# Optimization experiments

Hardware: AMD Instinct MI355X
Metric: run time of the kernel (lower is better)

## Reference

```python
import jax, jax.numpy as jnp
import numpy as np

EPS = 1e-4  # performer softmax-kernel stabilizer
LN_EPS = 1e-5


def _layernorm(x, g, b):
    m = jnp.mean(x, axis=-1, keepdims=True)
    v = jnp.mean(jnp.square(x - m), axis=-1, keepdims=True)
    return (x - m) * jax.lax.rsqrt(v + LN_EPS) * g + b


def _softmax_features(x, proj, is_query):
    # FAVOR+ positive softmax-kernel features. x: [B,H,N,Dh], proj: [M,Dh]
    d = x.shape[-1]
    xn = x * (d ** -0.25)                      # data normalizer d^{-1/4}
    u = jnp.einsum('bhnd,md->bhnm', xn, proj)  # [B,H,N,M]
    diag = 0.5 * jnp.sum(jnp.square(xn), axis=-1, keepdims=True)
    if is_query:
        stab = jnp.max(u, axis=-1, keepdims=True)
    else:
        stab = jnp.max(u, axis=(-2, -1), keepdims=True)
    ratio = proj.shape[0] ** -0.5
    return ratio * (jnp.exp(u - diag - stab) + EPS)


def reference(x, proj, ln1_g, ln1_b, ln2_g, ln2_b, W1, b1, W2, b2):
    B, N, E = x.shape
    M, Dh = proj.shape
    H = E // Dh

    # --- multi-head fast attention sublayer (pre-LN, q=k=v, no dropout) ---
    h = _layernorm(x, ln1_g, ln1_b)
    qkv = h.reshape(B, N, H, Dh).transpose(0, 2, 1, 3)     # [B,H,N,Dh]
    q_p = _softmax_features(qkv, proj, is_query=True)      # [B,H,N,M]
    k_p = _softmax_features(qkv, proj, is_query=False)     # [B,H,N,M]

    # non-causal linear attention: O(N*M*Dh)
    k_sum = jnp.sum(k_p, axis=-2)                          # [B,H,M]
    d_inv = 1.0 / jnp.einsum('bhnm,bhm->bhn', q_p, k_sum)  # [B,H,N]
    ctx = jnp.einsum('bhnm,bhnd->bhmd', k_p, qkv)          # [B,H,M,Dh]
    attn = jnp.einsum('bhnm,bhmd,bhn->bhnd', q_p, ctx, d_inv)
    attn = attn.transpose(0, 2, 1, 3).reshape(B, N, E)
    x = x + attn

    # --- MLP sublayer (pre-LN, GELU, dropout off in eval) ---
    h2 = _layernorm(x, ln2_g, ln2_b)
    h2 = jax.nn.gelu(h2 @ W1 + b1, approximate=False) @ W2 + b2
    return x + h2


def setup_inputs() -> dict:
    B, N, E, H, M, F = 4, 2048, 768, 12, 256, 3072
    Dh = E // H
    key = jax.random.key(0)
    ks = jax.random.split(key, 4)
    return {
        'x': jax.random.normal(ks[0], (B, N, E), jnp.float32),
        'proj': jax.random.normal(ks[1], (M, Dh), jnp.float32),
        'ln1_g': jnp.ones((E,), jnp.float32),
        'ln1_b': jnp.zeros((E,), jnp.float32),
        'ln2_g': jnp.ones((E,), jnp.float32),
        'ln2_b': jnp.zeros((E,), jnp.float32),
        'W1': jax.random.normal(ks[2], (E, F), jnp.float32) * 0.02,
        'b1': jnp.zeros((F,), jnp.float32),
        'W2': jax.random.normal(ks[3], (F, E), jnp.float32) * 0.02,
        'b2': jnp.zeros((E,), jnp.float32),
    }
```

## Files before the change

kernel.cpp:

```cpp
#include <hip/hip_runtime.h>
#include <hip/hip_bf16.h>
#include <math.h>

#define B_    4
#define N_    2048
#define E_    768
#define H_    12
#define M_    256
#define F_    3072
#define DH_   64
#define BN_   (B_ * N_)
#define BH_   (B_ * H_)
#define NSP_  16

#define EPS_F     1e-4f
#define LN_EPS_F  1e-5f
#define DNORM_F   0.35355339059327373f
#define DIAGC_F   0.0625f

typedef __attribute__((ext_vector_type(8))) short bf16x8;
typedef __attribute__((ext_vector_type(4))) float f32x4;

static __device__ __forceinline__ float to_f32(float v) { return v; }
static __device__ __forceinline__ float to_f32(__hip_bfloat16 v) { return __bfloat162float(v); }
static __device__ __forceinline__ short f2bf(float v) {
    __hip_bfloat16 b = __float2bfloat16(v);
    return *reinterpret_cast<short*>(&b);
}

static __device__ __forceinline__ float fast_gelu(float x) {
    float xc = fminf(fmaxf(x, -9.f), 9.f);
    float y = 0.7978845608028654f * (xc + 0.044715f * xc * xc * xc);
    float tt = __expf(-2.f * y);
    return x * __builtin_amdgcn_rcpf(1.f + tt);
}

static __device__ __forceinline__ void gld_lds16(const void* g, void* lds) {
    __builtin_amdgcn_global_load_lds((const __attribute__((address_space(1))) void*)g,
                                     (__attribute__((address_space(3))) void*)lds, 16, 0, 0);
}

__global__ void probe_kernel(const unsigned int* __restrict__ g1, int* __restrict__ flag) {
    if (threadIdx.x == 0 && blockIdx.x == 0)
        *flag = (*g1 == 0x3F803F80u) ? 1 : 0;
}

__global__ void convert_kernel(const void* __restrict__ src, __hip_bfloat16* __restrict__ dst,
                               int n, const int* __restrict__ flag) {
    int isb = *flag;
    int i = blockIdx.x * blockDim.x + threadIdx.x;
    int stride = gridDim.x * blockDim.x;
    if (isb) {
        const unsigned short* s = (const unsigned short*)src;
        unsigned short* d = (unsigned short*)dst;
        for (; i < n; i += stride) d[i] = s[i];
    } else {
        const float* s = (const float*)src;
        for (; i < n; i += stride) dst[i] = __float2bfloat16(s[i]);
    }
}

__global__ void convert_transpose_kernel(const void* __restrict__ src,
                                         __hip_bfloat16* __restrict__ dst,
                                         int R, int C, const int* __restrict__ flag) {
    __shared__ __hip_bfloat16 tile[32][33];
    int isb = *flag;
    int c0 = blockIdx.x * 32, r0 = blockIdx.y * 32;
    int tx = threadIdx.x & 31, ty = threadIdx.x >> 5;
    if (isb) {
        const unsigned short* s = (const unsigned short*)src;
        for (int j = 0; j < 4; ++j) {
            int r = ty + j * 8;
            ((unsigned short*)&tile[r][tx])[0] = s[(size_t)(r0 + r) * C + c0 + tx];
        }
    } else {
        const float* s = (const float*)src;
        for (int j = 0; j < 4; ++j) {
            int r = ty + j * 8;
            tile[r][tx] = __float2bfloat16(s[(size_t)(r0 + r) * C + c0 + tx]);
        }
    }
    __syncthreads();
    for (int j = 0; j < 4; ++j) {
        int r = ty + j * 8;
        dst[(size_t)(c0 + r) * R + r0 + tx] = tile[tx][r];
    }
}

template <typename TIn>
__global__ void ln_kernel(const TIn* __restrict__ x,
                          const __hip_bfloat16* __restrict__ g,
                          const __hip_bfloat16* __restrict__ b,
                          __hip_bfloat16* __restrict__ hout,
                          float* __restrict__ diag ) {
    int row = blockIdx.x;
    int t = threadIdx.x;
    __shared__ float rs[256], rq[256];
    __shared__ float hrow[E_];

    float xv[3];
    const TIn* xr = x + (size_t)row * E_;
    float s = 0.f, q = 0.f;
    for (int i = 0; i < 3; ++i) {
        xv[i] = to_f32(xr[t + i * 256]);
        s += xv[i];
        q += xv[i] * xv[i];
    }
    rs[t] = s; rq[t] = q;
    __syncthreads();
    for (int off = 128; off > 0; off >>= 1) {
        if (t < off) { rs[t] += rs[t + off]; rq[t] += rq[t + off]; }
        __syncthreads();
    }
    float mean = rs[0] * (1.0f / E_);
    float var  = rq[0] * (1.0f / E_) - mean * mean;
    float rinv = rsqrtf(fmaxf(var, 0.0f) + LN_EPS_F);

    __hip_bfloat16* hr = hout + (size_t)row * E_;
    for (int i = 0; i < 3; ++i) {
        int e = t + i * 256;
        float hv = (xv[i] - mean) * rinv * __bfloat162float(g[e]) + __bfloat162float(b[e]);
        hr[e] = __float2bfloat16(hv);
        hrow[e] = hv;
    }
    if (diag != nullptr) {
        __syncthreads();
        if (t < H_) {
            float acc = 0.f;
            for (int k = 0; k < DH_; ++k) { float v = hrow[t * DH_ + k]; acc += v * v; }
            diag[row * H_ + t] = DIAGC_F * acc;
        }
    }
}

__global__ __launch_bounds__(256) void ctx_mfma_kernel(
        const __hip_bfloat16* __restrict__ h,
        const __hip_bfloat16* __restrict__ proj,
        const float* __restrict__ diag,
        float* __restrict__ pctx, float* __restrict__ pksum,
        float* __restrict__ pmax, float* __restrict__ pvsum) {
    int sp = blockIdx.x, bh = blockIdx.y;
    int bb = bh / H_, hh = bh % H_;
    int n0 = sp * 128;
    int t = threadIdx.x, lane = t & 63, w = t >> 6;
    int lm = lane & 15, kg = lane >> 4;

    __shared__ __align__(16) short hv_s[128 * 72];
    __shared__ __align__(16) short vt_s[64 * 136];
    __shared__ __align__(16) short p_s[64 * 72];
    __shared__ __align__(16) short kpt_s[64 * 136];
    __shared__ float ksp_s[4][64];
    __shared__ float dg_s[128];
    __shared__ float wmax_s[4];
    __shared__ float vp_s[4][64];

    for (int it = 0; it < 4; ++it) {
        int c = t + it * 256; int n = c >> 3, kb = c & 7;
        uint4 vld = *(const uint4*)&h[((size_t)(bb * N_ + n0 + n)) * E_ + hh * DH_ + kb * 8];
        *(uint4*)&hv_s[n * 72 + kb * 8] = vld;
        union { uint4 u4; short sh[8]; } uu; uu.u4 = vld;
        for (int j = 0; j < 8; ++j) vt_s[(kb * 8 + j) * 136 + n] = uu.sh[j];
    }
    if (t < 128) dg_s[t] = diag[(size_t)(bb * N_ + n0 + t) * H_ + hh];
    __syncthreads();

    {
        int d = t & 63, rg = t >> 6;
        float s = 0.f;
        for (int n = rg * 32; n < rg * 32 + 32; ++n)
            s += __bfloat162float(*(const __hip_bfloat16*)&hv_s[n * 72 + d]);
        vp_s[rg][d] = s;
    }
    __syncthreads();
    if (t < 64)
        pvsum[((size_t)sp * BH_ + bh) * 64 + t] =
            vp_s[0][t] + vp_s[1][t] + vp_s[2][t] + vp_s[3][t];

    for (int q = 0; q < 4; ++q) {
        __syncthreads();
        for (int it = 0; it < 2; ++it) {
            int c = t + it * 256; int m = c >> 3, kb = c & 7;
            *(uint4*)&p_s[m * 72 + kb * 8] = *(const uint4*)&proj[(size_t)(q * 64 + m) * DH_ + kb * 8];
        }
        __syncthreads();

        f32x4 u[2][4];
        for (int i = 0; i < 2; ++i) for (int j = 0; j < 4; ++j) u[i][j] = (f32x4){0.f,0.f,0.f,0.f};
        for (int kc = 0; kc < 2; ++kc) {
            bf16x8 af[2], bf[4];
            for (int i = 0; i < 2; ++i)
                af[i] = *(const bf16x8*)&hv_s[(w * 32 + i * 16 + lm) * 72 + kc * 32 + kg * 8];
            for (int j = 0; j < 4; ++j)
                bf[j] = *(const bf16x8*)&p_s[(j * 16 + lm) * 72 + kc * 32 + kg * 8];
            for (int i = 0; i < 2; ++i)
                for (int j = 0; j < 4; ++j)
                    u[i][j] = __builtin_amdgcn_mfma_f32_16x16x32_bf16(af[i], bf[j], u[i][j], 0, 0, 0);
        }
        float lmax = -1e30f;
        for (int i = 0; i < 2; ++i) for (int j = 0; j < 4; ++j) for (int r = 0; r < 4; ++r) {
            u[i][j][r] *= DNORM_F;
            lmax = fmaxf(lmax, u[i][j][r]);
        }
        for (int off = 32; off >= 1; off >>= 1) lmax = fmaxf(lmax, __shfl_xor(lmax, off));
        if (lane == 0) wmax_s[w] = lmax;
        __syncthreads();
        float Lmax = fmaxf(fmaxf(wmax_s[0], wmax_s[1]), fmaxf(wmax_s[2], wmax_s[3]));

        float kpart[4] = {0.f, 0.f, 0.f, 0.f};
        for (int i = 0; i < 2; ++i) {
            float dgv[4];
            for (int r = 0; r < 4; ++r) dgv[r] = dg_s[w * 32 + i * 16 + kg * 4 + r];
            for (int j = 0; j < 4; ++j)
                for (int r = 0; r < 4; ++r) {
                    float val = expf(u[i][j][r] - dgv[r] - Lmax);
                    kpart[j] += val;
                    kpt_s[(j * 16 + lm) * 136 + (w * 32 + i * 16 + kg * 4 + r)] = f2bf(val);
                }
        }
        for (int j = 0; j < 4; ++j) {
            kpart[j] += __shfl_xor(kpart[j], 16);
            kpart[j] += __shfl_xor(kpart[j], 32);
        }
        if (lane < 16)
            for (int j = 0; j < 4; ++j) ksp_s[w][j * 16 + lm] = kpart[j];
        __syncthreads();

        f32x4 c4[4];
        for (int jd = 0; jd < 4; ++jd) c4[jd] = (f32x4){0.f,0.f,0.f,0.f};
        for (int kc = 0; kc < 4; ++kc) {
            bf16x8 a = *(const bf16x8*)&kpt_s[(w * 16 + lm) * 136 + kc * 32 + kg * 8];
            for (int jd = 0; jd < 4; ++jd) {
                bf16x8 b = *(const bf16x8*)&vt_s[(jd * 16 + lm) * 136 + kc * 32 + kg * 8];
                c4[jd] = __builtin_amdgcn_mfma_f32_16x16x32_bf16(a, b, c4[jd], 0, 0, 0);
            }
        }
        size_t base = ((size_t)sp * BH_ + bh) * M_ + q * 64 + w * 16;
        for (int jd = 0; jd < 4; ++jd)
            for (int r = 0; r < 4; ++r)
                pctx[(base + kg * 4 + r) * DH_ + jd * 16 + lm] = c4[jd][r];
        if (t < 64)
            pksum[((size_t)sp * BH_ + bh) * M_ + q * 64 + t] =
                ksp_s[0][t] + ksp_s[1][t] + ksp_s[2][t] + ksp_s[3][t];
        if (t == 0) pmax[bh * 64 + sp * 4 + q] = Lmax;
    }
}

__global__ void ctx_reduce_kernel(const float* __restrict__ pctx,
                                  const float* __restrict__ pksum,
                                  const float* __restrict__ pmax,
                                  const float* __restrict__ pvsum,
                                  __hip_bfloat16* __restrict__ ctx_t,
                                  float* __restrict__ ksum) {
    int mb = blockIdx.x, bh = blockIdx.y;
    int t = threadIdx.x;
    __shared__ float hm_s;
    __shared__ float sc_s[16];
    __shared__ float vs_s[64];
    __shared__ float tr_s[64 * 65];
    if (t < 64) {
        float v = pmax[bh * 64 + t];
        for (int off = 32; off >= 1; off >>= 1) v = fmaxf(v, __shfl_xor(v, off));
        if (t == 0) hm_s = v;
        float s = 0.f;
        for (int sp = 0; sp < 16; ++sp) s += pvsum[((size_t)sp * BH_ + bh) * 64 + t];
        vs_s[t] = s;
    }
    __syncthreads();
    if (t < 16) sc_s[t] = expf(pmax[bh * 64 + t * 4 + mb] - hm_s);
    __syncthreads();
    float scl[16];
    for (int sp = 0; sp < 16; ++sp) scl[sp] = sc_s[sp];
    int d = t & 63;
    for (int it = 0; it < 16; ++it) {
        int ml = (t >> 6) + it * 4;
        float acc = 0.f;
        for (int sp = 0; sp < 16; ++sp)
            acc += scl[sp] * pctx[(((size_t)sp * BH_ + bh) * M_ + mb * 64 + ml) * DH_ + d];
        tr_s[ml * 65 + d] = acc + EPS_F * vs_s[d];
    }
    if (t < 64) {
        float ka = 0.f;
        for (int sp = 0; sp < 16; ++sp)
            ka += scl[sp] * pksum[((size_t)sp * BH_ + bh) * M_ + mb * 64 + t];
        ksum[bh * M_ + mb * 64 + t] = ka + EPS_F * (float)N_;
    }
    __syncthreads();
    int mcol = t & 63;
    for (int jt = 0; jt < 16; ++jt) {
        int dl = (t >> 6) + jt * 4;
        ctx_t[((size_t)bh * DH_ + dl) * M_ + mb * 64 + mcol] = __float2bfloat16(tr_s[mcol * 65 + dl]);
    }
}

__global__ void sums_kernel(const __hip_bfloat16* __restrict__ ctx_t,
                            const float* __restrict__ ksum,
                            float* __restrict__ ctxsum, float* __restrict__ kssum) {
    int bh = blockIdx.x, t = threadIdx.x;
    __shared__ float red[256];
    int d = t >> 2, part = t & 3;
    float s = 0.f;
    for (int mm = part * 64; mm < part * 64 + 64; ++mm)
        s += __bfloat162float(ctx_t[((size_t)bh * DH_ + d) * M_ + mm]);
    red[t] = s;
    __syncthreads();
    if (t < 64) ctxsum[bh * 64 + t] = red[t * 4] + red[t * 4 + 1] + red[t * 4 + 2] + red[t * 4 + 3];
    __syncthreads();
    red[t] = ksum[bh * M_ + t];
    __syncthreads();
    for (int off = 128; off > 0; off >>= 1) {
        if (t < off) red[t] += red[t + off];
        __syncthreads();
    }
    if (t == 0) kssum[bh] = red[0];
}

__global__ __launch_bounds__(256) void attn_mfma_kernel(
        const __hip_bfloat16* __restrict__ h,
        const __hip_bfloat16* __restrict__ proj,
        const float* __restrict__ diag,
        const __hip_bfloat16* __restrict__ ctx_t,
        const float* __restrict__ ksum,
        const float* __restrict__ ctxsum,
        const float* __restrict__ kssum,
        const __hip_bfloat16* __restrict__ xin,
        float* __restrict__ x2) {
    int ntile = blockIdx.x, bh = blockIdx.y;
    int bb = bh / H_, hh = bh % H_;
    int n0 = ntile * 128;
    int t = threadIdx.x, lane = t & 63, w = t >> 6;
    int lm = lane & 15, kg = lane >> 4;

    __shared__ __align__(16) short hq_s[128 * 72];
    __shared__ __align__(16) short p_s[64 * 72];
    __shared__ __align__(16) short ct_s[64 * 72];
    __shared__ __align__(16) short qp_s[128 * 72];
    __shared__ float ksum_s[256];
    __shared__ float dg_s[128];
    __shared__ float cs_s[64];
    __shared__ float kss_s;

    for (int it = 0; it < 4; ++it) {
        int c = t + it * 256; int n = c >> 3, kb = c & 7;
        *(uint4*)&hq_s[n * 72 + kb * 8] =
            *(const uint4*)&h[((size_t)(bb * N_ + n0 + n)) * E_ + hh * DH_ + kb * 8];
    }
    if (t < 128) dg_s[t] = diag[(size_t)(bb * N_ + n0 + t) * H_ + hh];
    ksum_s[t] = ksum[bh * M_ + t];
    if (t < 64) cs_s[t] = ctxsum[bh * 64 + t];
    if (t == 0) kss_s = kssum[bh];

    f32x4 o[2][4];
    float qs[2][4], mrun[2][4];
    for (int i = 0; i < 2; ++i)
        for (int jd = 0; jd < 4; ++jd) o[i][jd] = (f32x4){0.f,0.f,0.f,0.f};
    for (int i = 0; i < 2; ++i)
        for (int r = 0; r < 4; ++r) { qs[i][r] = 0.f; mrun[i][r] = -1e30f; }

    for (int mc = 0; mc < 4; ++mc) {
        __syncthreads();
        for (int it = 0; it < 2; ++it) {
            int c = t + it * 256; int m = c >> 3, kb = c & 7;
            *(uint4*)&p_s[m * 72 + kb * 8] = *(const uint4*)&proj[(size_t)(mc * 64 + m) * DH_ + kb * 8];
            *(uint4*)&ct_s[m * 72 + kb * 8] =
                *(const uint4*)&ctx_t[((size_t)bh * DH_ + m) * M_ + mc * 64 + kb * 8];
        }
        __syncthreads();

        f32x4 u[2][4];
        for (int i = 0; i < 2; ++i) for (int j = 0; j < 4; ++j) u[i][j] = (f32x4){0.f,0.f,0.f,0.f};
        for (int kc = 0; kc < 2; ++kc) {
            bf16x8 af[2], bf[4];
            for (int i = 0; i < 2; ++i)
                af[i] = *(const bf16x8*)&hq_s[(w * 32 + i * 16 + lm) * 72 + kc * 32 + kg * 8];
            for (int j = 0; j < 4; ++j)
                bf[j] = *(const bf16x8*)&p_s[(j * 16 + lm) * 72 + kc * 32 + kg * 8];
            for (int i = 0; i < 2; ++i)
                for (int j = 0; j < 4; ++j)
                    u[i][j] = __builtin_amdgcn_mfma_f32_16x16x32_bf16(af[i], bf[j], u[i][j], 0, 0, 0);
        }
        for (int i = 0; i < 2; ++i) for (int j = 0; j < 4; ++j)
            for (int r = 0; r < 4; ++r) u[i][j][r] *= DNORM_F;

        for (int i = 0; i < 2; ++i)
            for (int r = 0; r < 4; ++r) {
                float cm = fmaxf(fmaxf(u[i][0][r], u[i][1][r]), fmaxf(u[i][2][r], u[i][3][r]));
                for (int off = 8; off >= 1; off >>= 1) cm = fmaxf(cm, __shfl_xor(cm, off));
                float mnew = fmaxf(mrun[i][r], cm);
                float sc = expf(mrun[i][r] - mnew);
                mrun[i][r] = mnew;
                qs[i][r] *= sc;
                for (int jd = 0; jd < 4; ++jd) o[i][jd][r] *= sc;
            }
        for (int i = 0; i < 2; ++i) {
            float dgv[4];
            for (int r = 0; r < 4; ++r) dgv[r] = dg_s[w * 32 + i * 16 + kg * 4 + r];
            for (int j = 0; j < 4; ++j) {
                float ksv = ksum_s[mc * 64 + j * 16 + lm];
                for (int r = 0; r < 4; ++r) {
                    float val = expf(u[i][j][r] - dgv[r] - mrun[i][r]);
                    qs[i][r] += val * ksv;
                    qp_s[(w * 32 + i * 16 + kg * 4 + r) * 72 + j * 16 + lm] = f2bf(val);
                }
            }
        }
        __syncthreads();
        for (int kc = 0; kc < 2; ++kc) {
            bf16x8 af[2], bf[4];
            for (int i = 0; i < 2; ++i)
                af[i] = *(const bf16x8*)&qp_s[(w * 32 + i * 16 + lm) * 72 + kc * 32 + kg * 8];
            for (int jd = 0; jd < 4; ++jd)
                bf[jd] = *(const bf16x8*)&ct_s[(jd * 16 + lm) * 72 + kc * 32 + kg * 8];
            for (int i = 0; i < 2; ++i)
                for (int jd = 0; jd < 4; ++jd)
                    o[i][jd] = __builtin_amdgcn_mfma_f32_16x16x32_bf16(af[i], bf[jd], o[i][jd], 0, 0, 0);
        }
    }

    for (int i = 0; i < 2; ++i)
        for (int r = 0; r < 4; ++r)
            for (int off = 8; off >= 1; off >>= 1) qs[i][r] += __shfl_xor(qs[i][r], off);
    float kss = kss_s;
    for (int i = 0; i < 2; ++i)
        for (int r = 0; r < 4; ++r) {
            float dinv = 1.0f / (qs[i][r] + EPS_F * kss);
            size_t row = (size_t)(bb * N_ + n0 + w * 32 + i * 16 + kg * 4 + r);
            for (int jd = 0; jd < 4; ++jd) {
                int dcol = jd * 16 + lm;
                float outv = (o[i][jd][r] + EPS_F * cs_s[dcol]) * dinv;
                int col = hh * DH_ + dcol;
                x2[row * E_ + col] = __bfloat162float(xin[row * E_ + col]) + outv;
            }
        }
}

template <int KK, int NCOLS, int TM, bool DO_GELU>
__global__ __launch_bounds__(256) void mfma_mlp_kernel(
        const __hip_bfloat16* __restrict__ A,
        const __hip_bfloat16* __restrict__ Bt,
        const __hip_bfloat16* __restrict__ bias,
        const float* __restrict__ resid,
        void* __restrict__ outv,
        const int* __restrict__ oflag) {
    constexpr int TN = 128;
    constexpr int WR = TM / 64;
    constexpr int WC = 4 / WR;
    constexpr int PW = TN / WC;
    constexpr int NB = PW / 16;
    constexpr int CA = TM / 16;
    constexpr int CB = TN / 16;
    constexpr int CPS = CA + CB;
    constexpr int CPW = CPS / 4;
    constexpr int LBUF = CPS * 512;
    constexpr int NT = KK / 32;

    const int t = threadIdx.x;
    const int col0 = blockIdx.x * TN;
    const int row0 = blockIdx.y * TM;
    const int lane = t & 63, w = t >> 6;
    const int wr = w % WR, wc = w / WR;
    const int lm = lane & 15, kg = lane >> 4;
    const int lr = lane >> 2, lc = (lane & 3) * 8;

    __shared__ __align__(16) short Ls[2 * LBUF];

    const __hip_bfloat16* gp[CPW];
    int lof[CPW];
#pragma unroll
    for (int cc = 0; cc < CPW; ++cc) {
        int c = w + cc * 4;
        gp[cc] = (c < CA) ? &A[(size_t)(row0 + c * 16 + lr) * KK + lc]
                          : &Bt[(size_t)(col0 + (c - CA) * 16 + lr) * KK + lc];
        lof[cc] = c * 512;
    }

    f32x4 acc[4][NB];
#pragma unroll
    for (int i = 0; i < 4; ++i)
#pragma unroll
        for (int j = 0; j < NB; ++j)
            acc[i][j] = (f32x4){0.f, 0.f, 0.f, 0.f};

#pragma unroll
    for (int cc = 0; cc < CPW; ++cc) gld_lds16(gp[cc], &Ls[lof[cc]]);
    __syncthreads();

    int buf = 0;
    for (int ts = 0; ts < NT; ++ts) {
        if (ts + 1 < NT) {
            const int nb_ = (buf ^ 1) * LBUF;
            const int ko = (ts + 1) * 32;
#pragma unroll
            for (int cc = 0; cc < CPW; ++cc)
                gld_lds16(gp[cc] + ko, &Ls[nb_ + lof[cc]]);
        }
        const short* base = &Ls[buf * LBUF];
        bf16x8 af[4], bfr[NB];
#pragma unroll
        for (int i = 0; i < 4; ++i)
            af[i] = *(const bf16x8*)&base[(wr * 64 + i * 16 + lm) * 32 + kg * 8];
#pragma unroll
        for (int j = 0; j < NB; ++j)
            bfr[j] = *(const bf16x8*)&base[(CA * 16 + wc * PW + j * 16 + lm) * 32 + kg * 8];
#pragma unroll
        for (int i = 0; i < 4; ++i)
#pragma unroll
            for (int j = 0; j < NB; ++j)
                acc[i][j] = __builtin_amdgcn_mfma_f32_16x16x32_bf16(af[i], bfr[j], acc[i][j], 0, 0, 0);
        __syncthreads();
        buf ^= 1;
    }

    int ob = DO_GELU ? 1 : *oflag;
#pragma unroll
    for (int i = 0; i < 4; ++i) {
#pragma unroll
        for (int r = 0; r < 4; ++r) {
            int row = row0 + wr * 64 + i * 16 + kg * 4 + r;
            size_t rb = (size_t)row * NCOLS;
#pragma unroll
            for (int j = 0; j < NB; ++j) {
                int col = col0 + wc * PW + j * 16 + lm;
                float v = acc[i][j][r] + __bfloat162float(bias[col]);
                if (DO_GELU) {
                    v = fast_gelu(v);
                } else {
                    v += resid[rb + col];
                }
                if (ob) ((__hip_bfloat16*)outv)[rb + col] = __float2bfloat16(v);
                else    ((float*)outv)[rb + col] = v;
            }
        }
    }
}

extern "C" void kernel_launch(void* const* d_in, const int* in_sizes, int n_in,
                              void* d_out, int out_size, void* d_ws, size_t ws_size,
                              hipStream_t stream) {
    char* ws = (char*)d_ws;
    size_t off = 0;
    auto carve = [&](size_t bytes) -> void* {
        void* p = ws + off;
        off += (bytes + 255) & ~(size_t)255;
        return p;
    };
    float*          x2    = (float*)carve((size_t)BN_ * E_ * 4);
    __hip_bfloat16* h     = (__hip_bfloat16*)carve((size_t)BN_ * E_ * 2);
    __hip_bfloat16* Wt1   = (__hip_bfloat16*)carve((size_t)E_ * F_ * 2);
    __hip_bfloat16* Wt2   = (__hip_bfloat16*)carve((size_t)F_ * E_ * 2);
    __hip_bfloat16* projc = (__hip_bfloat16*)carve((size_t)M_ * DH_ * 2);
    __hip_bfloat16* g1c   = (__hip_bfloat16*)carve((size_t)E_ * 2);
    __hip_bfloat16* b1lc  = (__hip_bfloat16*)carve((size_t)E_ * 2);
    __hip_bfloat16* g2c   = (__hip_bfloat16*)carve((size_t)E_ * 2);
    __hip_bfloat16* b2lc  = (__hip_bfloat16*)carve((size_t)E_ * 2);
    __hip_bfloat16* bb1c  = (__hip_bfloat16*)carve((size_t)F_ * 2);
    __hip_bfloat16* bb2c  = (__hip_bfloat16*)carve((size_t)E_ * 2);
    int*            flag  = (int*)carve(256);
    size_t mark = off;
    __hip_bfloat16* xc    = (__hip_bfloat16*)carve((size_t)BN_ * E_ * 2);
    float*          diag  = (float*)carve((size_t)BN_ * H_ * 4);
    float*          pctx  = (float*)carve((size_t)NSP_ * BH_ * M_ * DH_ * 4);
    float*          pksum = (float*)carve((size_t)NSP_ * BH_ * M_ * 4);
    float*          pmax  = (float*)carve((size_t)BH_ * 64 * 4);
    float*          pvsum = (float*)carve((size_t)NSP_ * BH_ * 64 * 4);
    __hip_bfloat16* ctx_t = (__hip_bfloat16*)carve((size_t)BH_ * DH_ * M_ * 2);
    float*          ksum  = (float*)carve((size_t)BH_ * M_ * 4);
    float*          ctxsum= (float*)carve((size_t)BH_ * DH_ * 4);
    float*          kssum = (float*)carve((size_t)BH_ * 4);
    __hip_bfloat16* h2    = h;
    __hip_bfloat16* mid   = (__hip_bfloat16*)(ws + mark);

    probe_kernel<<<1, 64, 0, stream>>>((const unsigned int*)d_in[2], flag);
    struct { const void* src; __hip_bfloat16* dst; int n; } cv[8] = {
        { d_in[0], xc,    BN_ * E_ },
        { d_in[1], projc, M_ * DH_ },
        { d_in[2], g1c,   E_ },
        { d_in[3], b1lc,  E_ },
        { d_in[4], g2c,   E_ },
        { d_in[5], b2lc,  E_ },
        { d_in[7], bb1c,  F_ },
        { d_in[9], bb2c,  E_ },
    };
    for (int i = 0; i < 8; ++i) {
        int blocks = (cv[i].n + 255) / 256; if (blocks > 1024) blocks = 1024;
        convert_kernel<<<blocks, 256, 0, stream>>>(cv[i].src, cv[i].dst, cv[i].n, flag);
    }
    convert_transpose_kernel<<<dim3(F_ / 32, E_ / 32), 256, 0, stream>>>(d_in[6], Wt1, E_, F_, flag);
    convert_transpose_kernel<<<dim3(E_ / 32, F_ / 32), 256, 0, stream>>>(d_in[8], Wt2, F_, E_, flag);

    ln_kernel<__hip_bfloat16><<<BN_, 256, 0, stream>>>(xc, g1c, b1lc, h, diag);
    ctx_mfma_kernel<<<dim3(NSP_, BH_), 256, 0, stream>>>(h, projc, diag, pctx, pksum, pmax, pvsum);
    ctx_reduce_kernel<<<dim3(4, BH_), 256, 0, stream>>>(pctx, pksum, pmax, pvsum, ctx_t, ksum);
    sums_kernel<<<BH_, 256, 0, stream>>>(ctx_t, ksum, ctxsum, kssum);
    attn_mfma_kernel<<<dim3(16, BH_), 256, 0, stream>>>(h, projc, diag, ctx_t, ksum, ctxsum, kssum, xc, x2);

    ln_kernel<float><<<BN_, 256, 0, stream>>>(x2, g2c, b2lc, h2, nullptr);
    mfma_mlp_kernel<E_, F_, 128, true><<<dim3(F_ / 128, BN_ / 128), 256, 0, stream>>>(
        h2, Wt1, bb1c, nullptr, (void*)mid, flag);
    mfma_mlp_kernel<F_, E_, 64, false><<<dim3(E_ / 128, BN_ / 64), 256, 0, stream>>>(
        mid, Wt2, bb2c, x2, d_out, flag);
}
```

Measured before the change: 402.7 us.

## Triple-buffer MLP GEMM LDS pipeline and swizzle workgroups across XCDs

The MLP GEMM kernel moves from a double-buffered LDS pipeline to a triple-buffered one that prefetches two K-steps ahead. It waits with explicit vmcnt and barriers instead of a full __syncthreads after each step, so global-to-LDS loads can overlap with MFMA work. Block IDs are also remapped so consecutive tiles land on the same XCD (8-way interleave), aiming for better L2 reuse. The cost is 1.5x the LDS per block, which may lower occupancy, plus extra barriers per iteration.

```diff
diff --git a/kernel.cpp b/kernel.cpp
--- a/kernel.cpp
+++ b/kernel.cpp
@@ -452,16 +452,22 @@
     constexpr int CPW = CPS / 4;
     constexpr int LBUF = CPS * 512;
     constexpr int NT = KK / 32;
+    constexpr int NXB = NCOLS / TN;
+    constexpr int NWG = NXB * (BN_ / TM);
+    constexpr int CPX = NWG / 8;
 
     const int t = threadIdx.x;
-    const int col0 = blockIdx.x * TN;
-    const int row0 = blockIdx.y * TM;
+    const int bid0 = blockIdx.y * NXB + blockIdx.x;
+    const int bid = (bid0 & 7) * CPX + (bid0 >> 3);
+    const int col0 = (bid % NXB) * TN;
+    const int row0 = (bid / NXB) * TM;
+
     const int lane = t & 63, w = t >> 6;
     const int wr = w % WR, wc = w / WR;
     const int lm = lane & 15, kg = lane >> 4;
     const int lr = lane >> 2, lc = (lane & 3) * 8;
 
-    __shared__ __align__(16) short Ls[2 * LBUF];
+    __shared__ __align__(16) short Ls[3 * LBUF];
 
     const __hip_bfloat16* gp[CPW];
     int lof[CPW];
@@ -482,18 +488,24 @@
 
 #pragma unroll
     for (int cc = 0; cc < CPW; ++cc) gld_lds16(gp[cc], &Ls[lof[cc]]);
-    __syncthreads();
-
-    int buf = 0;
+#pragma unroll
+    for (int cc = 0; cc < CPW; ++cc) gld_lds16(gp[cc] + 32, &Ls[LBUF + lof[cc]]);
+
+    int cur = 0;
     for (int ts = 0; ts < NT; ++ts) {
-        if (ts + 1 < NT) {
-            const int nb_ = (buf ^ 1) * LBUF;
-            const int ko = (ts + 1) * 32;
+        if (ts + 2 < NT) {
+            const int nb3 = (cur >= 1) ? (cur - 1) : 2;
+            const int ko = (ts + 2) * 32;
 #pragma unroll
             for (int cc = 0; cc < CPW; ++cc)
-                gld_lds16(gp[cc] + ko, &Ls[nb_ + lof[cc]]);
-        }
-        const short* base = &Ls[buf * LBUF];
+                gld_lds16(gp[cc] + ko, &Ls[nb3 * LBUF + lof[cc]]);
+        }
+        if (ts + 2 < NT)      asm volatile("s_waitcnt vmcnt(%0)" :: "n"(2 * CPW) : "memory");
+        else if (ts + 1 < NT) asm volatile("s_waitcnt vmcnt(%0)" :: "n"(CPW) : "memory");
+        else                  asm volatile("s_waitcnt vmcnt(0)" ::: "memory");
+        __builtin_amdgcn_s_barrier();
+
+        const short* base = &Ls[cur * LBUF];
         bf16x8 af[4], bfr[NB];
 #pragma unroll
         for (int i = 0; i < 4; ++i)
@@ -501,13 +513,17 @@
 #pragma unroll
         for (int j = 0; j < NB; ++j)
             bfr[j] = *(const bf16x8*)&base[(CA * 16 + wc * PW + j * 16 + lm) * 32 + kg * 8];
+
+        asm volatile("s_waitcnt lgkmcnt(0)" ::: "memory");
+        __builtin_amdgcn_sched_barrier(0);
+        __builtin_amdgcn_s_barrier();
+
 #pragma unroll
         for (int i = 0; i < 4; ++i)
 #pragma unroll
             for (int j = 0; j < NB; ++j)
                 acc[i][j] = __builtin_amdgcn_mfma_f32_16x16x32_bf16(af[i], bfr[j], acc[i][j], 0, 0, 0);
-        __syncthreads();
-        buf ^= 1;
+        cur = (cur == 2) ? 0 : (cur + 1);
     }
 
     int ob = DO_GELU ? 1 : *oflag;
```

New measurement: 394.1 us. 2.2% less time.
